# Kernel optimization log

Hardware: AMD Instinct MI355X
Metric: run time of the kernel (lower is better)

Reference implementation:

```python
import jax, jax.numpy as jnp
import numpy as np

NUM_HEADS = 8


def setup_inputs() -> dict:
    key = jax.random.key(0)
    k1, k2, k3 = jax.random.split(key, 3)
    B, N, C = 4, 2048, 256
    x = jax.random.normal(k1, (B, N, C), dtype=jnp.float32)
    qkv_w = jax.random.normal(k2, (3 * C, C), dtype=jnp.float32) * (C ** -0.5)
    proj_w = jax.random.normal(k3, (C, C), dtype=jnp.float32) * (C ** -0.5)
    proj_b = jnp.zeros((C,), dtype=jnp.float32)
    return {"x": x, "qkv_w": qkv_w, "proj_w": proj_w, "proj_b": proj_b}


def reference(x, qkv_w, proj_w, proj_b):
    B, N, C = x.shape
    H = NUM_HEADS
    hd = C // H
    scale = hd ** -0.5
    # 1x1 conv over [B,C,N,1] == per-token linear: [B,3C,N]
    qkv = jnp.einsum('bnc,dc->bdn', x, qkv_w)
    # faithful to torch reshape+chunk: per-head interleaved q/k/v layout
    qkv = qkv.reshape(B, H, 3 * hd, N)
    q, k, v = jnp.split(qkv, 3, axis=2)  # each [B,H,hd,N]
    # attn[b,h,i,j] = sum_d k[b,h,d,i] * q[b,h,d,j], scaled
    attn = jnp.einsum('bhdi,bhdj->bhij', k, q) * scale  # [B,H,Nk,Nq]
    attn = jax.nn.softmax(attn, axis=-2)  # softmax over key axis (dim=-2)
    out = jnp.einsum('bhdi,bhij->bhdj', v, attn)  # [B,H,hd,N]
    out = out.reshape(B, C, N, 1)
    # proj 1x1 conv with bias
    out = jnp.einsum('bcnq,dc->bdnq', out, proj_w) + proj_b[None, :, None, None]
    return out
```

## Files before the change

### kernel.cpp

```cpp
#include <hip/hip_runtime.h>
#include <hip/hip_bf16.h>

#define NTOK 2048
#define CDIM 256
#define HEADS 8
#define HD 32
#define SCALE 0.17677669529663687f

typedef __attribute__((ext_vector_type(8))) short short8;
typedef __attribute__((ext_vector_type(4))) float float4v;
typedef unsigned short ushort_t;
typedef unsigned int uint_t;

#define MFMA(a, b, c) __builtin_amdgcn_mfma_f32_16x16x32_bf16(a, b, c, 0, 0, 0)

__device__ __forceinline__ uint_t cvt_pk(float lo, float hi) {
    uint_t r;
    asm("v_cvt_pk_bf16_f32 %0, %1, %2" : "=v"(r) : "v"(lo), "v"(hi));
    return r;
}
__device__ __forceinline__ ushort_t f2bf(float f) {
    union { __hip_bfloat16 h; ushort_t u; } cv;
    cv.h = __float2bfloat16(f);
    return cv.u;
}

__global__ __launch_bounds__(256) void cvt_bf16(const float* __restrict__ in,
                                                uint4* __restrict__ out, int n8) {
    int i = blockIdx.x * 256 + threadIdx.x;
    if (i >= n8) return;
    const float4* p = (const float4*)in + (size_t)2 * i;
    float4 a = p[0], bq = p[1];
    uint4 r;
    r.x = cvt_pk(a.x, a.y);  r.y = cvt_pk(a.z, a.w);
    r.z = cvt_pk(bq.x, bq.y); r.w = cvt_pk(bq.z, bq.w);
    out[i] = r;
}

__global__ __launch_bounds__(256) void qkv_mfma(const ushort_t* __restrict__ x_bf,
                                                const ushort_t* __restrict__ w_bf,
                                                ushort_t* __restrict__ q_t,
                                                ushort_t* __restrict__ k_t,
                                                ushort_t* __restrict__ v_) {
    const int tid = threadIdx.x, wave = tid >> 6, lane = tid & 63;
    const int l15 = lane & 15, g = lane >> 4;
    const int b = blockIdx.z;
    const int dtile = blockIdx.x * 64 + (wave >> 1) * 32;
    const int ntile = blockIdx.y * 128 + (wave & 1) * 64;

    const ushort_t* A = w_bf + (size_t)dtile * CDIM + g * 8;
    const ushort_t* B = x_bf + ((size_t)b * NTOK + ntile) * CDIM + g * 8;

    float4v acc[2][4];
    #pragma unroll
    for (int i = 0; i < 2; ++i)
        #pragma unroll
        for (int j = 0; j < 4; ++j)
            #pragma unroll
            for (int r = 0; r < 4; ++r) acc[i][j][r] = 0.f;

    #pragma unroll
    for (int k0 = 0; k0 < CDIM; k0 += 32) {
        short8 af[2], bf[4];
        #pragma unroll
        for (int i = 0; i < 2; ++i)
            af[i] = *(const short8*)&A[(size_t)(l15 + 16 * i) * CDIM + k0];
        #pragma unroll
        for (int j = 0; j < 4; ++j)
            bf[j] = *(const short8*)&B[(size_t)(l15 + 16 * j) * CDIM + k0];
        #pragma unroll
        for (int i = 0; i < 2; ++i)
            #pragma unroll
            for (int j = 0; j < 4; ++j)
                acc[i][j] = MFMA(af[i], bf[j], acc[i][j]);
    }

    const int hq = (dtile * 683) >> 16;
    const int tl = dtile - hq * 96;
    const size_t bh = (size_t)(b * HEADS + hq);

    if (tl == 64) {
        #pragma unroll
        for (int i = 0; i < 2; ++i)
            #pragma unroll
            for (int j = 0; j < 4; ++j)
                #pragma unroll
                for (int r = 0; r < 4; ++r)
                    v_[bh * ((size_t)NTOK * HD) + (size_t)(i * 16 + g * 4 + r) * NTOK
                       + ntile + j * 16 + l15] = f2bf(acc[i][j][r]);
    } else {
        ushort_t* base = (tl ? k_t : q_t) + bh * ((size_t)NTOK * HD);
        const float mul = tl ? 1.f : SCALE;
        #pragma unroll
        for (int i = 0; i < 2; ++i)
            #pragma unroll
            for (int j = 0; j < 4; ++j) {
                uint2 pk;
                pk.x = cvt_pk(acc[i][j][0] * mul, acc[i][j][1] * mul);
                pk.y = cvt_pk(acc[i][j][2] * mul, acc[i][j][3] * mul);
                *(uint2*)&base[(size_t)(ntile + j * 16 + l15) * HD + i * 16 + g * 4] = pk;
            }
    }
}

__global__ __launch_bounds__(256) void attn_mfma(const ushort_t* __restrict__ q_t,
                                                 const ushort_t* __restrict__ k_t,
                                                 const ushort_t* __restrict__ v_,
                                                 ushort_t* __restrict__ preT) {
    __shared__ uint_t pt[4][2][16 * 20];
    __shared__ float comb[4][64][18];
    const int tid = threadIdx.x, wave = tid >> 6, lane = tid & 63;
    const int l15 = lane & 15, g = lane >> 4;
    const int bh = blockIdx.x, b = bh >> 3, h = bh & 7;
    const int j0 = blockIdx.y * 64 + (wave >> 1) * 32;
    const int khalf = wave & 1;

    const ushort_t* qb = q_t + (size_t)bh * (NTOK * HD);
    const ushort_t* kb = k_t + (size_t)bh * (NTOK * HD);
    const ushort_t* vb = v_  + (size_t)bh * (NTOK * HD);

    short8 qf0 = *(const short8*)&qb[(size_t)(j0 + l15) * HD + g * 8];
    short8 qf1 = *(const short8*)&qb[(size_t)(j0 + 16 + l15) * HD + g * 8];

    const float4v z4 = {0.f, 0.f, 0.f, 0.f};
    float4v o00 = z4, o01 = z4, o10 = z4, o11 = z4;
    float lsum0 = 0.f, lsum1 = 0.f;

    uint_t* pt0 = &pt[wave][0][0];
    uint_t* pt1 = &pt[wave][1][0];
    const int wbase = l15 * 20 + g * 2;
    const int rbase = l15 * 20 + g * 4;

    const int kbeg = khalf * 1024, kend = kbeg + 1024;
    for (int i0 = kbeg; i0 < kend; i0 += 32) {
        short8 aK0 = *(const short8*)&kb[(size_t)(i0 + l15) * HD + g * 8];
        short8 aK1 = *(const short8*)&kb[(size_t)(i0 + 16 + l15) * HD + g * 8];

        float4v s00 = MFMA(aK0, qf0, z4);
        float4v s10 = MFMA(aK1, qf0, z4);
        float4v s01 = MFMA(aK0, qf1, z4);
        float4v s11 = MFMA(aK1, qf1, z4);

        {
            float e0[4], e1[4];
            #pragma unroll
            for (int r = 0; r < 4; ++r) { e0[r] = __expf(s00[r]); e1[r] = __expf(s10[r]); }
            lsum0 += e0[0]+e0[1]+e0[2]+e0[3] + e1[0]+e1[1]+e1[2]+e1[3];
            pt0[wbase]     = cvt_pk(e0[0], e0[1]);
            pt0[wbase + 1] = cvt_pk(e0[2], e0[3]);
            pt0[wbase + 8] = cvt_pk(e1[0], e1[1]);
            pt0[wbase + 9] = cvt_pk(e1[2], e1[3]);
        }
        {
            float e0[4], e1[4];
            #pragma unroll
            for (int r = 0; r < 4; ++r) { e0[r] = __expf(s01[r]); e1[r] = __expf(s11[r]); }
            lsum1 += e0[0]+e0[1]+e0[2]+e0[3] + e1[0]+e1[1]+e1[2]+e1[3];
            pt1[wbase]     = cvt_pk(e0[0], e0[1]);
            pt1[wbase + 1] = cvt_pk(e0[2], e0[3]);
            pt1[wbase + 8] = cvt_pk(e1[0], e1[1]);
            pt1[wbase + 9] = cvt_pk(e1[2], e1[3]);
        }

        short8 pB0 = *(const short8*)&pt0[rbase];
        short8 pB1 = *(const short8*)&pt1[rbase];

        short8 aV0 = *(const short8*)&vb[(size_t)l15 * NTOK + i0 + g * 8];
        short8 aV1 = *(const short8*)&vb[(size_t)(16 + l15) * NTOK + i0 + g * 8];

        o00 = MFMA(aV0, pB0, o00);
        o01 = MFMA(aV0, pB1, o01);
        o10 = MFMA(aV1, pB0, o10);
        o11 = MFMA(aV1, pB1, o11);
    }

    lsum0 += __shfl_xor(lsum0, 16, 64); lsum0 += __shfl_xor(lsum0, 32, 64);
    lsum1 += __shfl_xor(lsum1, 16, 64); lsum1 += __shfl_xor(lsum1, 32, 64);

    float* cb = &comb[wave][lane][0];
    #pragma unroll
    for (int r = 0; r < 4; ++r) {
        cb[r] = o00[r]; cb[4 + r] = o01[r]; cb[8 + r] = o10[r]; cb[12 + r] = o11[r];
    }
    cb[16] = lsum0; cb[17] = lsum1;
    __syncthreads();

    if (khalf == 0) {
        const float* cp = &comb[wave ^ 1][lane][0];
        #pragma unroll
        for (int r = 0; r < 4; ++r) {
            o00[r] += cp[r]; o01[r] += cp[4 + r]; o10[r] += cp[8 + r]; o11[r] += cp[12 + r];
        }
        const float rl0 = 1.f / (lsum0 + cp[16]);
        const float rl1 = 1.f / (lsum1 + cp[17]);

        ushort_t* pb_ = preT + ((size_t)b * NTOK + j0) * CDIM + h * HD;
        uint2 w0, w1, w2, w3;
        w0.x = cvt_pk(o00[0] * rl0, o00[1] * rl0); w0.y = cvt_pk(o00[2] * rl0, o00[3] * rl0);
        w1.x = cvt_pk(o01[0] * rl1, o01[1] * rl1); w1.y = cvt_pk(o01[2] * rl1, o01[3] * rl1);
        w2.x = cvt_pk(o10[0] * rl0, o10[1] * rl0); w2.y = cvt_pk(o10[2] * rl0, o10[3] * rl0);
        w3.x = cvt_pk(o11[0] * rl1, o11[1] * rl1); w3.y = cvt_pk(o11[2] * rl1, o11[3] * rl1);
        *(uint2*)&pb_[(size_t)l15 * CDIM + g * 4] = w0;
        *(uint2*)&pb_[(size_t)(16 + l15) * CDIM + g * 4] = w1;
        *(uint2*)&pb_[(size_t)l15 * CDIM + 16 + g * 4] = w2;
        *(uint2*)&pb_[(size_t)(16 + l15) * CDIM + 16 + g * 4] = w3;
    }
}

__global__ __launch_bounds__(256) void proj_mfma(const ushort_t* __restrict__ preT,
                                                 const ushort_t* __restrict__ w2_bf,
                                                 const float* __restrict__ pb,
                                                 float* __restrict__ out) {
    const int tid = threadIdx.x, wave = tid >> 6, lane = tid & 63;
    const int l15 = lane & 15, g = lane >> 4;
    const int b = blockIdx.z;
    const int dtile = blockIdx.x * 64 + (wave >> 1) * 32;
    const int ntile = blockIdx.y * 64 + (wave & 1) * 32;

    const ushort_t* A = w2_bf + (size_t)dtile * CDIM + g * 8;
    const ushort_t* B = preT + ((size_t)b * NTOK + ntile) * CDIM + g * 8;

    float4v acc[2][2];
    #pragma unroll
    for (int i = 0; i < 2; ++i)
        #pragma unroll
        for (int j = 0; j < 2; ++j)
            #pragma unroll
            for (int r = 0; r < 4; ++r) acc[i][j][r] = 0.f;

    #pragma unroll
    for (int k0 = 0; k0 < CDIM; k0 += 32) {
        short8 af[2], bf[2];
        #pragma unroll
        for (int i = 0; i < 2; ++i)
            af[i] = *(const short8*)&A[(size_t)(l15 + 16 * i) * CDIM + k0];
        #pragma unroll
        for (int j = 0; j < 2; ++j)
            bf[j] = *(const short8*)&B[(size_t)(l15 + 16 * j) * CDIM + k0];
        #pragma unroll
        for (int i = 0; i < 2; ++i)
            #pragma unroll
            for (int j = 0; j < 2; ++j)
                acc[i][j] = MFMA(af[i], bf[j], acc[i][j]);
    }

    #pragma unroll
    for (int i = 0; i < 2; ++i) {
        #pragma unroll
        for (int r = 0; r < 4; ++r) {
            const int d = dtile + i * 16 + g * 4 + r;
            const float bias = pb[d];
            float* orow = out + ((size_t)b * CDIM + d) * NTOK + ntile;
            #pragma unroll
            for (int j = 0; j < 2; ++j)
                orow[j * 16 + l15] = acc[i][j][r] + bias;
        }
    }
}

extern "C" void kernel_launch(void* const* d_in, const int* in_sizes, int n_in,
                              void* d_out, int out_size, void* d_ws, size_t ws_size,
                              hipStream_t stream) {
    const float* x      = (const float*)d_in[0];
    const float* qkv_w  = (const float*)d_in[1];
    const float* proj_w = (const float*)d_in[2];
    const float* proj_b = (const float*)d_in[3];
    float* out = (float*)d_out;

    char* ws = (char*)d_ws;
    ushort_t* x_bf  = (ushort_t*)(ws);
    ushort_t* preT  = (ushort_t*)(ws);
    ushort_t* w_bf  = (ushort_t*)(ws + (size_t)4 * 1024 * 1024);
    ushort_t* w2_bf = (ushort_t*)(ws + (size_t)4608 * 1024);
    ushort_t* q_t   = (ushort_t*)(ws + (size_t)5 * 1024 * 1024);
    ushort_t* k_t   = (ushort_t*)(ws + (size_t)9 * 1024 * 1024);
    ushort_t* v_    = (ushort_t*)(ws + (size_t)13 * 1024 * 1024);

    cvt_bf16<<<1024, 256, 0, stream>>>(x,      (uint4*)x_bf,  262144);
    cvt_bf16<<<96,   256, 0, stream>>>(qkv_w,  (uint4*)w_bf,  24576);
    cvt_bf16<<<32,   256, 0, stream>>>(proj_w, (uint4*)w2_bf, 8192);
    qkv_mfma<<<dim3(12, 16, 4), 256, 0, stream>>>(x_bf, w_bf, q_t, k_t, v_);
    attn_mfma<<<dim3(4 * HEADS, NTOK / 64), 256, 0, stream>>>(q_t, k_t, v_, preT);
    proj_mfma<<<dim3(4, 32, 4), 256, 0, stream>>>(preT, w2_bf, proj_b, out);
}
```

Measured before the change: 148.6 us.

## Fuse conversion kernels, stage QKV stores through LDS, exp2 softmax, MFMA row sums, prefetch K/V

Merges the three bf16 conversion launches into one kernel. QKV outputs are staged through XOR-swizzled LDS so global stores become coalesced 16-byte writes instead of scattered 2-byte or 8-byte ones. The attention kernel folds log2(e) into the Q scale so it can use native exp2, and computes softmax denominators with an MFMA against a ones vector instead of scalar adds and shuffles. K/V loads are software-prefetched one iteration ahead. The cost is extra LDS, more registers, and a redundant wraparound prefetch on the last iteration.

New measurement: 144.8 us. 1.03x faster.

```diff
diff --git a/kernel.cpp b/kernel.cpp
--- a/kernel.cpp
+++ b/kernel.cpp
@@ -5,7 +5,7 @@
 #define CDIM 256
 #define HEADS 8
 #define HD 32
-#define SCALE 0.17677669529663687f
+#define QSC 0.25505480068568306f
 
 typedef __attribute__((ext_vector_type(8))) short short8;
 typedef __attribute__((ext_vector_type(4))) float float4v;
@@ -24,15 +24,27 @@
     cv.h = __float2bfloat16(f);
     return cv.u;
 }
-
-__global__ __launch_bounds__(256) void cvt_bf16(const float* __restrict__ in,
-                                                uint4* __restrict__ out, int n8) {
-    int i = blockIdx.x * 256 + threadIdx.x;
-    if (i >= n8) return;
+#if __has_builtin(__builtin_amdgcn_exp2f)
+#define EXP2(x) __builtin_amdgcn_exp2f(x)
+#else
+#define EXP2(x) exp2f(x)
+#endif
+
+__global__ __launch_bounds__(256) void cvt_all(const float* __restrict__ x,
+                                               const float* __restrict__ w,
+                                               const float* __restrict__ w2,
+                                               uint4* __restrict__ xo,
+                                               uint4* __restrict__ wo,
+                                               uint4* __restrict__ w2o) {
+    const int bid = blockIdx.x;
+    const float* in; uint4* out; int i;
+    if (bid < 1024)      { in = x;  out = xo;  i = bid * 256 + threadIdx.x; }
+    else if (bid < 1120) { in = w;  out = wo;  i = (bid - 1024) * 256 + threadIdx.x; }
+    else                 { in = w2; out = w2o; i = (bid - 1120) * 256 + threadIdx.x; }
     const float4* p = (const float4*)in + (size_t)2 * i;
     float4 a = p[0], bq = p[1];
     uint4 r;
-    r.x = cvt_pk(a.x, a.y);  r.y = cvt_pk(a.z, a.w);
+    r.x = cvt_pk(a.x, a.y);   r.y = cvt_pk(a.z, a.w);
     r.z = cvt_pk(bq.x, bq.y); r.w = cvt_pk(bq.z, bq.w);
     out[i] = r;
 }
@@ -42,6 +54,7 @@
                                                 ushort_t* __restrict__ q_t,
                                                 ushort_t* __restrict__ k_t,
                                                 ushort_t* __restrict__ v_) {
+    __shared__ ushort_t lds[4][2048];
     const int tid = threadIdx.x, wave = tid >> 6, lane = tid & 63;
     const int l15 = lane & 15, g = lane >> 4;
     const int b = blockIdx.z;
@@ -78,19 +91,30 @@
     const int hq = (dtile * 683) >> 16;
     const int tl = dtile - hq * 96;
     const size_t bh = (size_t)(b * HEADS + hq);
+    ushort_t* W = lds[wave];
 
     if (tl == 64) {
         #pragma unroll
         for (int i = 0; i < 2; ++i)
             #pragma unroll
-            for (int j = 0; j < 4; ++j)
+            for (int j = 0; j < 4; ++j) {
+                const int c = j * 2 + (l15 >> 3);
                 #pragma unroll
-                for (int r = 0; r < 4; ++r)
-                    v_[bh * ((size_t)NTOK * HD) + (size_t)(i * 16 + g * 4 + r) * NTOK
-                       + ntile + j * 16 + l15] = f2bf(acc[i][j][r]);
+                for (int r = 0; r < 4; ++r) {
+                    const int d = i * 16 + g * 4 + r;
+                    W[d * 64 + ((c ^ (d & 7)) * 8) + (l15 & 7)] = f2bf(acc[i][j][r]);
+                }
+            }
+        ushort_t* vb = v_ + bh * ((size_t)NTOK * HD);
+        #pragma unroll
+        for (int t = 0; t < 4; ++t) {
+            const int d = t * 8 + (lane >> 3), c = lane & 7;
+            uint4 val = *(const uint4*)&W[d * 64 + ((c ^ (d & 7)) * 8)];
+            *(uint4*)&vb[(size_t)d * NTOK + ntile + c * 8] = val;
+        }
     } else {
         ushort_t* base = (tl ? k_t : q_t) + bh * ((size_t)NTOK * HD);
-        const float mul = tl ? 1.f : SCALE;
+        const float mul = tl ? 1.f : QSC;
         #pragma unroll
         for (int i = 0; i < 2; ++i)
             #pragma unroll
@@ -98,8 +122,16 @@
                 uint2 pk;
                 pk.x = cvt_pk(acc[i][j][0] * mul, acc[i][j][1] * mul);
                 pk.y = cvt_pk(acc[i][j][2] * mul, acc[i][j][3] * mul);
-                *(uint2*)&base[(size_t)(ntile + j * 16 + l15) * HD + i * 16 + g * 4] = pk;
+                const int row = j * 16 + l15;
+                const int c16 = i * 2 + (g >> 1);
+                *(uint2*)&W[row * 32 + ((c16 ^ (row & 3)) * 8) + (g & 1) * 4] = pk;
             }
+        #pragma unroll
+        for (int t = 0; t < 4; ++t) {
+            const int row = t * 16 + (lane >> 2), c = lane & 3;
+            uint4 val = *(const uint4*)&W[row * 32 + ((c ^ (row & 3)) * 8)];
+            *(uint4*)&base[(size_t)(ntile + row) * HD + c * 8] = val;
+        }
     }
 }
 
@@ -107,8 +139,7 @@
                                                  const ushort_t* __restrict__ k_t,
                                                  const ushort_t* __restrict__ v_,
                                                  ushort_t* __restrict__ preT) {
-    __shared__ uint_t pt[4][2][16 * 20];
-    __shared__ float comb[4][64][18];
+    __shared__ float smem[4][1152];
     const int tid = threadIdx.x, wave = tid >> 6, lane = tid & 63;
     const int l15 = lane & 15, g = lane >> 4;
     const int bh = blockIdx.x, b = bh >> 3, h = bh & 7;
@@ -122,77 +153,81 @@
     short8 qf0 = *(const short8*)&qb[(size_t)(j0 + l15) * HD + g * 8];
     short8 qf1 = *(const short8*)&qb[(size_t)(j0 + 16 + l15) * HD + g * 8];
 
+    short8 ones;
+    #pragma unroll
+    for (int r = 0; r < 8; ++r) ones[r] = (short)0x3F80;
+
     const float4v z4 = {0.f, 0.f, 0.f, 0.f};
     float4v o00 = z4, o01 = z4, o10 = z4, o11 = z4;
-    float lsum0 = 0.f, lsum1 = 0.f;
-
-    uint_t* pt0 = &pt[wave][0][0];
-    uint_t* pt1 = &pt[wave][1][0];
+    float4v lacc0 = z4, lacc1 = z4;
+
+    float* myb = smem[wave];
+    uint_t* pt0 = (uint_t*)myb;
+    uint_t* pt1 = (uint_t*)myb + 320;
     const int wbase = l15 * 20 + g * 2;
     const int rbase = l15 * 20 + g * 4;
 
     const int kbeg = khalf * 1024, kend = kbeg + 1024;
+    short8 aK0 = *(const short8*)&kb[(size_t)(kbeg + l15) * HD + g * 8];
+    short8 aK1 = *(const short8*)&kb[(size_t)(kbeg + 16 + l15) * HD + g * 8];
+    short8 aV0 = *(const short8*)&vb[(size_t)l15 * NTOK + kbeg + g * 8];
+    short8 aV1 = *(const short8*)&vb[(size_t)(16 + l15) * NTOK + kbeg + g * 8];
+
     for (int i0 = kbeg; i0 < kend; i0 += 32) {
-        short8 aK0 = *(const short8*)&kb[(size_t)(i0 + l15) * HD + g * 8];
-        short8 aK1 = *(const short8*)&kb[(size_t)(i0 + 16 + l15) * HD + g * 8];
+        const int ip = (i0 + 32 < kend) ? i0 + 32 : kbeg;
+        short8 nK0 = *(const short8*)&kb[(size_t)(ip + l15) * HD + g * 8];
+        short8 nK1 = *(const short8*)&kb[(size_t)(ip + 16 + l15) * HD + g * 8];
+        short8 nV0 = *(const short8*)&vb[(size_t)l15 * NTOK + ip + g * 8];
+        short8 nV1 = *(const short8*)&vb[(size_t)(16 + l15) * NTOK + ip + g * 8];
 
         float4v s00 = MFMA(aK0, qf0, z4);
         float4v s10 = MFMA(aK1, qf0, z4);
         float4v s01 = MFMA(aK0, qf1, z4);
         float4v s11 = MFMA(aK1, qf1, z4);
 
-        {
-            float e0[4], e1[4];
-            #pragma unroll
-            for (int r = 0; r < 4; ++r) { e0[r] = __expf(s00[r]); e1[r] = __expf(s10[r]); }
-            lsum0 += e0[0]+e0[1]+e0[2]+e0[3] + e1[0]+e1[1]+e1[2]+e1[3];
-            pt0[wbase]     = cvt_pk(e0[0], e0[1]);
-            pt0[wbase + 1] = cvt_pk(e0[2], e0[3]);
-            pt0[wbase + 8] = cvt_pk(e1[0], e1[1]);
-            pt0[wbase + 9] = cvt_pk(e1[2], e1[3]);
-        }
-        {
-            float e0[4], e1[4];
-            #pragma unroll
-            for (int r = 0; r < 4; ++r) { e0[r] = __expf(s01[r]); e1[r] = __expf(s11[r]); }
-            lsum1 += e0[0]+e0[1]+e0[2]+e0[3] + e1[0]+e1[1]+e1[2]+e1[3];
-            pt1[wbase]     = cvt_pk(e0[0], e0[1]);
-            pt1[wbase + 1] = cvt_pk(e0[2], e0[3]);
-            pt1[wbase + 8] = cvt_pk(e1[0], e1[1]);
-            pt1[wbase + 9] = cvt_pk(e1[2], e1[3]);
-        }
+        uint2 w0, w1;
+        w0.x = cvt_pk(EXP2(s00[0]), EXP2(s00[1]));
+        w0.y = cvt_pk(EXP2(s00[2]), EXP2(s00[3]));
+        w1.x = cvt_pk(EXP2(s10[0]), EXP2(s10[1]));
+        w1.y = cvt_pk(EXP2(s10[2]), EXP2(s10[3]));
+        *(uint2*)&pt0[wbase]     = w0;
+        *(uint2*)&pt0[wbase + 8] = w1;
+        w0.x = cvt_pk(EXP2(s01[0]), EXP2(s01[1]));
+        w0.y = cvt_pk(EXP2(s01[2]), EXP2(s01[3]));
+        w1.x = cvt_pk(EXP2(s11[0]), EXP2(s11[1]));
+        w1.y = cvt_pk(EXP2(s11[2]), EXP2(s11[3]));
+        *(uint2*)&pt1[wbase]     = w0;
+        *(uint2*)&pt1[wbase + 8] = w1;
 
         short8 pB0 = *(const short8*)&pt0[rbase];
         short8 pB1 = *(const short8*)&pt1[rbase];
 
-        short8 aV0 = *(const short8*)&vb[(size_t)l15 * NTOK + i0 + g * 8];
-        short8 aV1 = *(const short8*)&vb[(size_t)(16 + l15) * NTOK + i0 + g * 8];
-
+        lacc0 = MFMA(ones, pB0, lacc0);
+        lacc1 = MFMA(ones, pB1, lacc1);
         o00 = MFMA(aV0, pB0, o00);
         o01 = MFMA(aV0, pB1, o01);
         o10 = MFMA(aV1, pB0, o10);
         o11 = MFMA(aV1, pB1, o11);
-    }
-
-    lsum0 += __shfl_xor(lsum0, 16, 64); lsum0 += __shfl_xor(lsum0, 32, 64);
-    lsum1 += __shfl_xor(lsum1, 16, 64); lsum1 += __shfl_xor(lsum1, 32, 64);
-
-    float* cb = &comb[wave][lane][0];
+
+        aK0 = nK0; aK1 = nK1; aV0 = nV0; aV1 = nV1;
+    }
+
+    float* dst = &myb[lane * 18];
     #pragma unroll
     for (int r = 0; r < 4; ++r) {
-        cb[r] = o00[r]; cb[4 + r] = o01[r]; cb[8 + r] = o10[r]; cb[12 + r] = o11[r];
-    }
-    cb[16] = lsum0; cb[17] = lsum1;
+        dst[r] = o00[r]; dst[4 + r] = o01[r]; dst[8 + r] = o10[r]; dst[12 + r] = o11[r];
+    }
+    dst[16] = lacc0[0]; dst[17] = lacc1[0];
     __syncthreads();
 
     if (khalf == 0) {
-        const float* cp = &comb[wave ^ 1][lane][0];
+        const float* cp = &smem[wave ^ 1][lane * 18];
         #pragma unroll
         for (int r = 0; r < 4; ++r) {
             o00[r] += cp[r]; o01[r] += cp[4 + r]; o10[r] += cp[8 + r]; o11[r] += cp[12 + r];
         }
-        const float rl0 = 1.f / (lsum0 + cp[16]);
-        const float rl1 = 1.f / (lsum1 + cp[17]);
+        const float rl0 = 1.f / (lacc0[0] + cp[16]);
+        const float rl1 = 1.f / (lacc1[0] + cp[17]);
 
         ushort_t* pb_ = preT + ((size_t)b * NTOK + j0) * CDIM + h * HD;
         uint2 w0, w1, w2, w3;
@@ -276,9 +311,8 @@
     ushort_t* k_t   = (ushort_t*)(ws + (size_t)9 * 1024 * 1024);
     ushort_t* v_    = (ushort_t*)(ws + (size_t)13 * 1024 * 1024);
 
-    cvt_bf16<<<1024, 256, 0, stream>>>(x,      (uint4*)x_bf,  262144);
-    cvt_bf16<<<96,   256, 0, stream>>>(qkv_w,  (uint4*)w_bf,  24576);
-    cvt_bf16<<<32,   256, 0, stream>>>(proj_w, (uint4*)w2_bf, 8192);
+    cvt_all<<<1152, 256, 0, stream>>>(x, qkv_w, proj_w,
+                                      (uint4*)x_bf, (uint4*)w_bf, (uint4*)w2_bf);
     qkv_mfma<<<dim3(12, 16, 4), 256, 0, stream>>>(x_bf, w_bf, q_t, k_t, v_);
     attn_mfma<<<dim3(4 * HEADS, NTOK / 64), 256, 0, stream>>>(q_t, k_t, v_, preT);
     proj_mfma<<<dim3(4, 32, 4), 256, 0, stream>>>(preT, w2_bf, proj_b, out);
```
